# Optimization experiments

Measured on AMD Instinct MI355X. Metric: run time of the kernel, lower is better.

## Reference

```python
import jax, jax.numpy as jnp
import numpy as np

TEMPERATURE = 1.0 / 13.544


def setup_inputs() -> dict:
    key = jax.random.key(0)
    x = jax.random.normal(key, (8, 2048, 128), dtype=jnp.float32)
    return {"x": x, "is_batch_mode": 1}


def reference(x, is_batch_mode):
    # batched pairwise squared-L2 distance via norm expansion:
    # d[b,i,j] = ||x_i||^2 - 2 x_i . x_j + ||x_j||^2
    sq = jnp.sum(x * x, axis=-1)                       # [B, N]
    dots = jnp.einsum('bnd,bmd->bnm', x, x)            # [B, N, N]
    dist = sq[:, :, None] - 2.0 * dots + sq[:, None, :]
    dist = jnp.maximum(dist, 0.0)
    sim = jax.nn.softmax(-TEMPERATURE * dist, axis=-1)  # [B, N, N]
    return sim[..., None]                               # [B, N, N, 1]
```

## Files before the change

kernel.cpp:

```cpp
#include <hip/hip_runtime.h>
#include <hip/hip_bf16.h>
#include <cstdint>


using bf16x8 = __attribute__((ext_vector_type(8))) short;
using f32x4  = __attribute__((ext_vector_type(4))) float;

#define TEMP   (1.0f / 13.544f)
#define LOG2E  1.4426950408889634f

__global__ __launch_bounds__(256) void prep_kernel(
    const float* __restrict__ x, uint4* __restrict__ xbf, float* __restrict__ csq)
{
    const int t   = threadIdx.x;
    const int lr  = t >> 4;
    const int q   = t & 15;
    const int row = blockIdx.x * 16 + lr;

    const float* xp = x + (size_t)row * 128 + q * 8;
    float4 a0 = *(const float4*)(xp);
    float4 a1 = *(const float4*)(xp + 4);
    float v[8] = {a0.x, a0.y, a0.z, a0.w, a1.x, a1.y, a1.z, a1.w};

    unsigned u[8];
    float s = 0.f;
#pragma unroll
    for (int e = 0; e < 8; ++e) {
        unsigned ui = __float_as_uint(v[e]);
        unsigned r  = (ui + 0x7FFFu + ((ui >> 16) & 1u)) >> 16;
        u[e] = r;
        float d = __uint_as_float(r << 16);
        s += d * d;
    }
    uint4 pack;
    pack.x = u[0] | (u[1] << 16);
    pack.y = u[2] | (u[3] << 16);
    pack.z = u[4] | (u[5] << 16);
    pack.w = u[6] | (u[7] << 16);

    const int b  = row >> 11;
    const int g  = (row >> 4) & 127;
    const int rr = row & 15;
    xbf[(b * 128 + g) * 256 + q * 16 + rr] = pack;

#pragma unroll
    for (int m = 1; m < 16; m <<= 1) s += __shfl_xor(s, m, 64);
    if (q == 0) csq[row] = s * (-TEMP * LOG2E);
}

__global__ __launch_bounds__(256, 2) void sim_kernel(
    const uint4* __restrict__ xbf, const float* __restrict__ csq, float* __restrict__ out)
{
    const int blk  = blockIdx.x;
    const int b    = blk & 7;
    const int i0   = (blk >> 3) * 16;
    const int tid  = threadIdx.x;
    const int w    = tid >> 6;
    const int lane = tid & 63;
    const int quad = lane >> 4;
    const int l15  = lane & 15;

    __shared__ __align__(16) char lsP[4][8192];
    __shared__ float lsSum[4][16];
    __shared__ __align__(16) float lsInv[16];

    const uint4* xbb  = xbf + (size_t)b * (128 * 256);
    const float* csqb = csq + b * 2048;

    bf16x8 afrag[4];
#pragma unroll
    for (int k4 = 0; k4 < 4; ++k4) {
        uint4 vv = xbb[(i0 >> 4) * 256 + (k4 * 4 + quad) * 16 + l15];
        afrag[k4] = __builtin_bit_cast(bf16x8, vv);
    }

    const float csqi = csqb[i0 + l15];
    const float C2L  = 2.0f * TEMP * LOG2E;
    const int   c0   = w * 32;

    f32x4 P0[16], P1[16];
    float sum_ = 0.f;
#pragma unroll
    for (int jt = 0; jt < 16; ++jt) {
        const int j0 = jt * 128;
        float4 cj0 = *(const float4*)(csqb + j0 + c0 + quad * 4);
        float4 cj1 = *(const float4*)(csqb + j0 + c0 + 16 + quad * 4);

        const uint4* b0p = xbb + (size_t)(jt * 8 + w * 2 + 0) * 256 + quad * 16 + l15;
        const uint4* b1p = b0p + 256;

        f32x4 acc[2] = {};
#pragma unroll
        for (int k4 = 0; k4 < 4; ++k4) {
            bf16x8 b0 = __builtin_bit_cast(bf16x8, b0p[k4 * 64]);
            bf16x8 b1 = __builtin_bit_cast(bf16x8, b1p[k4 * 64]);
            acc[0] = __builtin_amdgcn_mfma_f32_16x16x32_bf16(b0, afrag[k4], acc[0], 0, 0, 0);
            acc[1] = __builtin_amdgcn_mfma_f32_16x16x32_bf16(b1, afrag[k4], acc[1], 0, 0, 0);
        }

        f32x4 p0, p1;
        p0[0] = exp2f(fminf(fmaf(C2L, acc[0][0], csqi + cj0.x), 0.f));
        p0[1] = exp2f(fminf(fmaf(C2L, acc[0][1], csqi + cj0.y), 0.f));
        p0[2] = exp2f(fminf(fmaf(C2L, acc[0][2], csqi + cj0.z), 0.f));
        p0[3] = exp2f(fminf(fmaf(C2L, acc[0][3], csqi + cj0.w), 0.f));
        p1[0] = exp2f(fminf(fmaf(C2L, acc[1][0], csqi + cj1.x), 0.f));
        p1[1] = exp2f(fminf(fmaf(C2L, acc[1][1], csqi + cj1.y), 0.f));
        p1[2] = exp2f(fminf(fmaf(C2L, acc[1][2], csqi + cj1.z), 0.f));
        p1[3] = exp2f(fminf(fmaf(C2L, acc[1][3], csqi + cj1.w), 0.f));
        P0[jt] = p0;
        P1[jt] = p1;
        sum_ += p0[0] + p0[1] + p0[2] + p0[3] + p1[0] + p1[1] + p1[2] + p1[3];
    }

    sum_ += __shfl_xor(sum_, 16, 64);
    sum_ += __shfl_xor(sum_, 32, 64);
    if (quad == 0) lsSum[w][l15] = sum_;
    __syncthreads();
    if (tid < 16) {
        lsInv[tid] = 1.0f / (lsSum[0][tid] + lsSum[1][tid] + lsSum[2][tid] + lsSum[3][tid]);
    }
    __syncthreads();
    const float inv = lsInv[l15];

    const int wr   = l15 << 9;
    const int ws   = (l15 & 7) << 4;
    const int wc0  = (c0 << 2) + (quad << 4);
    const int c32  = (lane & 31) << 4;
    const int half = lane >> 5;
    char* obase = (char*)(out + ((size_t)b * 2048 + i0) * 2048);

#pragma unroll
    for (int rd = 0; rd < 4; ++rd) {
#pragma unroll
        for (int t4 = 0; t4 < 4; ++t4) {
            const int jt = rd * 4 + t4;
            char* buf = lsP[t4];
            f32x4 s0 = P0[jt] * inv;
            f32x4 s1 = P1[jt] * inv;
            *(f32x4*)(buf + wr + ((wc0)      ^ ws)) = s0;
            *(f32x4*)(buf + wr + ((wc0 + 64) ^ ws)) = s1;
        }
        __syncthreads();
#pragma unroll
        for (int r4 = 0; r4 < 4; ++r4) {
            const int row = w * 4 + r4;
            const int swz = (row & 7) << 4;
#pragma unroll
            for (int seg = 0; seg < 2; ++seg) {
                const char* buf = lsP[seg * 2 + half];
                f32x4 v = *(const f32x4*)(buf + (row << 9) + (c32 ^ swz));
                *(f32x4*)(obase + (size_t)row * 8192 + rd * 2048 + seg * 1024 + (lane << 4)) = v;
            }
        }
        __syncthreads();
    }
}

extern "C" void kernel_launch(void* const* d_in, const int* in_sizes, int n_in,
                              void* d_out, int out_size, void* d_ws, size_t ws_size,
                              hipStream_t stream) {
    const float* x   = (const float*)d_in[0];
    float*       out = (float*)d_out;
    uint4* xbf = (uint4*)d_ws;
    float* csq = (float*)((char*)d_ws + (size_t)4 * 1024 * 1024);

    prep_kernel<<<1024, 256, 0, stream>>>(x, xbf, csq);
    sim_kernel<<<1024, 256, 0, stream>>>(xbf, csq, out);
}
```

Before: 156.7 us.

## Split sim_kernel column range across two wave groups with 512-thread blocks

Doubles the block to 512 threads (8 waves), with two groups of four waves each handling half of the 2048 columns. This halves the per-thread register arrays holding softmax numerators, which should raise occupancy and latency hiding. The store phase is reorganized so each thread writes 512-byte row segments from shared-memory tiles. The costs are a cross-group reduction over 8 partial sums and more waves sharing the same block barriers.

```diff
diff --git a/kernel.cpp b/kernel.cpp
--- a/kernel.cpp
+++ b/kernel.cpp
@@ -48,7 +48,7 @@
     if (q == 0) csq[row] = s * (-TEMP * LOG2E);
 }
 
-__global__ __launch_bounds__(256, 2) void sim_kernel(
+__global__ __launch_bounds__(512, 4) void sim_kernel(
     const uint4* __restrict__ xbf, const float* __restrict__ csq, float* __restrict__ out)
 {
     const int blk  = blockIdx.x;
@@ -56,12 +56,13 @@
     const int i0   = (blk >> 3) * 16;
     const int tid  = threadIdx.x;
     const int w    = tid >> 6;
+    const int g    = w >> 2;
     const int lane = tid & 63;
     const int quad = lane >> 4;
     const int l15  = lane & 15;
 
     __shared__ __align__(16) char lsP[4][8192];
-    __shared__ float lsSum[4][16];
+    __shared__ float lsSum[8][16];
     __shared__ __align__(16) float lsInv[16];
 
     const uint4* xbb  = xbf + (size_t)b * (128 * 256);
@@ -76,17 +77,18 @@
 
     const float csqi = csqb[i0 + l15];
     const float C2L  = 2.0f * TEMP * LOG2E;
-    const int   c0   = w * 32;
+    const int   cw   = (w & 3) * 32;
 
-    f32x4 P0[16], P1[16];
+    f32x4 P0[8], P1[8];
     float sum_ = 0.f;
 #pragma unroll
-    for (int jt = 0; jt < 16; ++jt) {
+    for (int lt = 0; lt < 8; ++lt) {
+        const int jt = g * 8 + lt;
         const int j0 = jt * 128;
-        float4 cj0 = *(const float4*)(csqb + j0 + c0 + quad * 4);
-        float4 cj1 = *(const float4*)(csqb + j0 + c0 + 16 + quad * 4);
+        float4 cj0 = *(const float4*)(csqb + j0 + cw + quad * 4);
+        float4 cj1 = *(const float4*)(csqb + j0 + cw + 16 + quad * 4);
 
-        const uint4* b0p = xbb + (size_t)(jt * 8 + w * 2 + 0) * 256 + quad * 16 + l15;
+        const uint4* b0p = xbb + (size_t)(jt * 8 + (w & 3) * 2) * 256 + quad * 16 + l15;
         const uint4* b1p = b0p + 256;
 
         f32x4 acc[2] = {};
@@ -107,8 +109,8 @@
         p1[1] = exp2f(fminf(fmaf(C2L, acc[1][1], csqi + cj1.y), 0.f));
         p1[2] = exp2f(fminf(fmaf(C2L, acc[1][2], csqi + cj1.z), 0.f));
         p1[3] = exp2f(fminf(fmaf(C2L, acc[1][3], csqi + cj1.w), 0.f));
-        P0[jt] = p0;
-        P1[jt] = p1;
+        P0[lt] = p0;
+        P1[lt] = p1;
         sum_ += p0[0] + p0[1] + p0[2] + p0[3] + p1[0] + p1[1] + p1[2] + p1[3];
     }
 
@@ -117,39 +119,44 @@
     if (quad == 0) lsSum[w][l15] = sum_;
     __syncthreads();
     if (tid < 16) {
-        lsInv[tid] = 1.0f / (lsSum[0][tid] + lsSum[1][tid] + lsSum[2][tid] + lsSum[3][tid]);
+        float tot = 0.f;
+#pragma unroll
+        for (int k = 0; k < 8; ++k) tot += lsSum[k][tid];
+        lsInv[tid] = 1.0f / tot;
     }
     __syncthreads();
     const float inv = lsInv[l15];
 
     const int wr   = l15 << 9;
     const int ws   = (l15 & 7) << 4;
-    const int wc0  = (c0 << 2) + (quad << 4);
-    const int c32  = (lane & 31) << 4;
-    const int half = lane >> 5;
+    const int wc0  = (cw << 2) + (quad << 4);
+    const int tb   = tid >> 7;
+    const int rr   = (tid >> 3) & 15;
+    const int cc   = (tid & 7) << 4;
+    const int rsw  = (rr & 7) << 4;
     char* obase = (char*)(out + ((size_t)b * 2048 + i0) * 2048);
 
 #pragma unroll
     for (int rd = 0; rd < 4; ++rd) {
 #pragma unroll
-        for (int t4 = 0; t4 < 4; ++t4) {
-            const int jt = rd * 4 + t4;
-            char* buf = lsP[t4];
-            f32x4 s0 = P0[jt] * inv;
-            f32x4 s1 = P1[jt] * inv;
+        for (int q = 0; q < 2; ++q) {
+            const int lt = rd * 2 + q;
+            char* buf = lsP[g * 2 + q];
+            f32x4 s0 = P0[lt] * inv;
+            f32x4 s1 = P1[lt] * inv;
             *(f32x4*)(buf + wr + ((wc0)      ^ ws)) = s0;
             *(f32x4*)(buf + wr + ((wc0 + 64) ^ ws)) = s1;
         }
         __syncthreads();
+        {
+            const int jt = rd * 2 + (tb & 1) + 8 * (tb >> 1);
+            const char* buf = lsP[tb];
+            char* orow = obase + (size_t)rr * 8192 + jt * 512;
 #pragma unroll
-        for (int r4 = 0; r4 < 4; ++r4) {
-            const int row = w * 4 + r4;
-            const int swz = (row & 7) << 4;
-#pragma unroll
-            for (int seg = 0; seg < 2; ++seg) {
-                const char* buf = lsP[seg * 2 + half];
-                f32x4 v = *(const f32x4*)(buf + (row << 9) + (c32 ^ swz));
-                *(f32x4*)(obase + (size_t)row * 8192 + rd * 2048 + seg * 1024 + (lane << 4)) = v;
+            for (int pass = 0; pass < 4; ++pass) {
+                const int bc = cc + pass * 128;
+                f32x4 v = *(const f32x4*)(buf + (rr << 9) + (bc ^ rsw));
+                *(f32x4*)(orow + bc) = v;
             }
         }
         __syncthreads();
@@ -165,5 +172,5 @@
     float* csq = (float*)((char*)d_ws + (size_t)4 * 1024 * 1024);
 
     prep_kernel<<<1024, 256, 0, stream>>>(x, xbf, csq);
-    sim_kernel<<<1024, 256, 0, stream>>>(xbf, csq, out);
+    sim_kernel<<<1024, 512, 0, stream>>>(xbf, csq, out);
 }
```

After: 161.5 us. +3.1%, slower.
